# Kernel optimization log

Measured on AMD Instinct MI355X. Metric: run time of the kernel, lower is better.

The kernel has to match this reference:

```python
import jax, jax.numpy as jnp
import numpy as np

ROI = 7
NMS_THR = 0.01
NMS_SIZE = 100


def crop_and_resize(fmap, boxes, crop):
    # fmap [H,W,C], boxes [N,4] normalized (y1,x1,y2,x2) -> [N,crop,crop,C]
    H, W, C = fmap.shape
    t = jnp.linspace(0.0, 1.0, crop)
    ys = (boxes[:, 0:1] + (boxes[:, 2:3] - boxes[:, 0:1]) * t) * (H - 1)  # [N,crop]
    xs = (boxes[:, 1:2] + (boxes[:, 3:4] - boxes[:, 1:2]) * t) * (W - 1)
    y0 = jnp.clip(jnp.floor(ys), 0, H - 1).astype(jnp.int32)
    x0 = jnp.clip(jnp.floor(xs), 0, W - 1).astype(jnp.int32)
    y1 = jnp.clip(y0 + 1, 0, H - 1)
    x1 = jnp.clip(x0 + 1, 0, W - 1)
    wy = (ys - y0)[:, :, None, None]
    wx = (xs - x0)[:, None, :, None]
    Y0, Y1 = y0[:, :, None], y1[:, :, None]
    X0, X1 = x0[:, None, :], x1[:, None, :]
    f00 = fmap[Y0, X0]; f01 = fmap[Y0, X1]
    f10 = fmap[Y1, X0]; f11 = fmap[Y1, X1]
    return (f00 * (1 - wy) * (1 - wx) + f01 * (1 - wy) * wx
            + f10 * wy * (1 - wx) + f11 * wy * wx)


def iou_matrix(b):
    # b [N,4] (x1,y1,x2,y2)
    area = jnp.maximum(b[:, 2] - b[:, 0], 0) * jnp.maximum(b[:, 3] - b[:, 1], 0)
    lt = jnp.maximum(b[:, None, :2], b[None, :, :2])
    rb = jnp.minimum(b[:, None, 2:], b[None, :, 2:])
    wh = jnp.maximum(rb - lt, 0.0)
    inter = wh[..., 0] * wh[..., 1]
    return inter / (area[:, None] + area[None, :] - inter + 1e-8)


def nms(boxes, scores, thr, max_out):
    # greedy NMS, fixed-size output (pads with lowest-ranked boxes when fewer survive)
    N = boxes.shape[0]
    order = jnp.argsort(-scores)
    M = iou_matrix(boxes[order])
    idx = jnp.arange(N)
    def body(i, keep):
        sup = (M[i] > thr) & (idx > i) & keep[i]
        return keep & ~sup
    keep = jax.lax.fori_loop(0, N, body, jnp.ones(N, dtype=bool))
    rank = jnp.where(keep, idx, N + idx)
    sel = jnp.argsort(rank)[:max_out]
    return order[sel]


def make_boxes(key, n):
    kc, ks = jax.random.split(key)
    c = jax.random.uniform(kc, (n, 2), minval=0.1, maxval=0.9)
    s = jax.random.uniform(ks, (n, 2), minval=0.02, maxval=0.15)
    lo = jnp.clip(c - s / 2, 0.0, 1.0)
    hi = jnp.clip(c + s / 2, 0.0, 1.0)
    return jnp.concatenate([lo, hi], axis=1)  # (y1,x1,y2,x2)


def setup_inputs() -> dict:
    key = jax.random.key(0)
    ks = jax.random.split(key, 12)
    N, D, Hd = 1024, ROI * ROI * 32, 2048
    img_boxes = make_boxes(ks[0], N)
    bev_boxes = make_boxes(ks[1], N)
    bev_boxes_abs = bev_boxes[:, jnp.array([1, 0, 3, 2])] * 80.0  # (x1,y1,x2,y2) in meters
    def w(k, shape, fan_in):
        return jax.random.normal(k, shape, jnp.float32) * (2.0 / fan_in) ** 0.5
    return {
        'img_feat_map': jax.random.uniform(ks[2], (1, 360, 1200, 32), jnp.float32),
        'bev_feat_map': jax.random.uniform(ks[3], (1, 700, 800, 32), jnp.float32),
        'img_boxes': img_boxes,
        'bev_boxes': bev_boxes,
        'bev_boxes_abs': bev_boxes_abs,
        'img_mask': jnp.ones((1, 1, 1, 1), jnp.float32),
        'bev_mask': jnp.ones((1, 1, 1, 1), jnp.float32),
        'W1': w(ks[4], (D, Hd), D), 'b1': jnp.zeros((Hd,), jnp.float32),
        'W2': w(ks[5], (Hd, Hd), Hd), 'b2': jnp.zeros((Hd,), jnp.float32),
        'Wc': w(ks[6], (Hd, 2), Hd), 'bc': jnp.zeros((2,), jnp.float32),
        'Wo': w(ks[7], (Hd, 10), Hd), 'bo': jnp.zeros((10,), jnp.float32),
        'Wa': w(ks[8], (Hd, 2), Hd), 'ba': jnp.zeros((2,), jnp.float32),
    }


def reference(img_feat_map, bev_feat_map, img_boxes, bev_boxes, bev_boxes_abs,
              img_mask, bev_mask, W1, b1, W2, b2, Wc, bc, Wo, bo, Wa, ba):
    # ROI align on masked feature maps
    rois_rgb = crop_and_resize((img_mask * img_feat_map)[0], img_boxes, ROI)
    rois_bev = crop_and_resize((bev_mask * bev_feat_map)[0], bev_boxes, ROI)
    # mean fusion
    fused = (rois_rgb + rois_bev) / (img_mask + bev_mask)  # [N,7,7,32]
    # predictor
    x = fused.reshape(fused.shape[0], -1)
    h = jax.nn.relu(x @ W1 + b1)
    h = jax.nn.relu(h @ W2 + b2)
    obj = h @ Wc + bc            # [N,2]
    off = h @ Wo + bo            # [N,10]
    ang = h @ Wa + ba            # [N,2]
    obj_soft = jax.nn.softmax(obj, axis=1)
    orient = jnp.arctan2(ang[:, 1], ang[:, 0])  # convert_angle_to_orientation
    # offset-adjusted BEV boxes for NMS
    pb = bev_boxes_abs + 0.1 * off[:, :4]
    boxes = jnp.stack([jnp.minimum(pb[:, 0], pb[:, 2]), jnp.minimum(pb[:, 1], pb[:, 3]),
                       jnp.maximum(pb[:, 0], pb[:, 2]), jnp.maximum(pb[:, 1], pb[:, 3])], axis=1)
    scores = jnp.max(obj[:, 1:], axis=1)
    ti = nms(jax.lax.stop_gradient(boxes), jax.lax.stop_gradient(scores), NMS_THR, NMS_SIZE)
    # [100, 2 + 4 + 1]: softmax scores, pred bev boxes, orientations
    return jnp.concatenate([obj_soft[ti], boxes[ti], orient[ti][:, None]], axis=1)
```

## Files before the change

### kernel.cpp

```cpp
#include <hip/hip_runtime.h>
#include <math.h>

#define NBOX 1024
#define ROI_N 7
#define CH 32
#define FEAT (ROI_N*ROI_N*CH)
#define K1PAD 1600
#define HD 2048
#define NMS_THR_F 0.01f
#define NMS_OUT 100
#define MTRI_WORDS 8704

typedef _Float16 f16;
typedef f16 f16x8 __attribute__((ext_vector_type(8)));
typedef float f32x4 __attribute__((ext_vector_type(4)));

__device__ __forceinline__ void split_f16(float v, f16& h, f16& l) {
  h = (f16)v;
  l = (f16)((v - (float)h) * 4096.0f);
}

__global__ __launch_bounds__(256) void roi_fuse_kernel(
    const float* __restrict__ img, const float* __restrict__ bev,
    const float* __restrict__ img_boxes, const float* __restrict__ bev_boxes,
    const float* __restrict__ img_mask, const float* __restrict__ bev_mask,
    f16* __restrict__ xh, f16* __restrict__ xl)
{
  const int b = blockIdx.x;
  const float mi = img_mask[0], mb = bev_mask[0];
  const float denom = mi + mb;

  const float iy0 = img_boxes[b*4+0], ix0 = img_boxes[b*4+1];
  const float iy1 = img_boxes[b*4+2], ix1 = img_boxes[b*4+3];
  const float by0 = bev_boxes[b*4+0], bx0 = bev_boxes[b*4+1];
  const float by1 = bev_boxes[b*4+2], bx1 = bev_boxes[b*4+3];

  for (int idx = threadIdx.x; idx < K1PAD; idx += 256) {
    if (idx >= FEAT) {
      xh[(size_t)b*K1PAD + idx] = (f16)0.0f;
      xl[(size_t)b*K1PAD + idx] = (f16)0.0f;
      continue;
    }
    const int ti  = idx / (ROI_N*CH);
    const int rem = idx - ti*(ROI_N*CH);
    const int tj  = rem >> 5;
    const int c   = rem & 31;
    const float tt_i = (ti == ROI_N-1) ? 1.0f : ti * (1.0f/(ROI_N-1));
    const float tt_j = (tj == ROI_N-1) ? 1.0f : tj * (1.0f/(ROI_N-1));

    float vi, vb;
    {
      const int H = 360, W = 1200;
      const float ys = (iy0 + (iy1 - iy0) * tt_i) * (float)(H-1);
      const float xs = (ix0 + (ix1 - ix0) * tt_j) * (float)(W-1);
      int y0 = (int)floorf(ys); y0 = y0 < 0 ? 0 : (y0 > H-1 ? H-1 : y0);
      int x0 = (int)floorf(xs); x0 = x0 < 0 ? 0 : (x0 > W-1 ? W-1 : x0);
      const int y1 = (y0+1 > H-1) ? H-1 : y0+1;
      const int x1 = (x0+1 > W-1) ? W-1 : x0+1;
      const float wy = ys - (float)y0;
      const float wx = xs - (float)x0;
      const float f00 = img[(y0*W + x0)*CH + c];
      const float f01 = img[(y0*W + x1)*CH + c];
      const float f10 = img[(y1*W + x0)*CH + c];
      const float f11 = img[(y1*W + x1)*CH + c];
      vi = f00*(1.0f-wy)*(1.0f-wx) + f01*(1.0f-wy)*wx
         + f10*wy*(1.0f-wx)        + f11*wy*wx;
    }
    {
      const int H = 700, W = 800;
      const float ys = (by0 + (by1 - by0) * tt_i) * (float)(H-1);
      const float xs = (bx0 + (bx1 - bx0) * tt_j) * (float)(W-1);
      int y0 = (int)floorf(ys); y0 = y0 < 0 ? 0 : (y0 > H-1 ? H-1 : y0);
      int x0 = (int)floorf(xs); x0 = x0 < 0 ? 0 : (x0 > W-1 ? W-1 : x0);
      const int y1 = (y0+1 > H-1) ? H-1 : y0+1;
      const int x1 = (x0+1 > W-1) ? W-1 : x0+1;
      const float wy = ys - (float)y0;
      const float wx = xs - (float)x0;
      const float f00 = bev[(y0*W + x0)*CH + c];
      const float f01 = bev[(y0*W + x1)*CH + c];
      const float f10 = bev[(y1*W + x0)*CH + c];
      const float f11 = bev[(y1*W + x1)*CH + c];
      vb = f00*(1.0f-wy)*(1.0f-wx) + f01*(1.0f-wy)*wx
         + f10*wy*(1.0f-wx)        + f11*wy*wx;
    }
    f16 h, l;
    split_f16((mi*vi + mb*vb) / denom, h, l);
    xh[(size_t)b*K1PAD + idx] = h;
    xl[(size_t)b*K1PAD + idx] = l;
  }
}

__global__ __launch_bounds__(256) void convt_w_kernel(
    const float* __restrict__ W, f16* __restrict__ Wt_hi, f16* __restrict__ Wt_lo,
    int K, int Kpad, int N)
{
  __shared__ float t[64][33];
  const int tid = threadIdx.x;
  const int n0 = blockIdx.x * 32, k0 = blockIdx.y * 64;
#pragma unroll
  for (int p = 0; p < 8; ++p) {
    const int idx = tid + p*256;
    const int kk = idx >> 5, nn = idx & 31;
    const int k = k0 + kk;
    t[kk][nn] = (k < K) ? W[(size_t)k*N + n0 + nn] : 0.0f;
  }
  __syncthreads();
  const int nn = tid >> 3;
  const int kg = (tid & 7) * 8;
  f16x8 h8, l8;
#pragma unroll
  for (int q = 0; q < 8; ++q) {
    const float v = t[kg + q][nn];
    f16 h, l;
    split_f16(v, h, l);
    h8[q] = h; l8[q] = l;
  }
  *(f16x8*)&Wt_hi[(size_t)(n0+nn)*Kpad + k0 + kg] = h8;
  *(f16x8*)&Wt_lo[(size_t)(n0+nn)*Kpad + k0 + kg] = l8;
}

#define LOADG(KK)                                                              \
  do {                                                                         \
    _Pragma("unroll")                                                          \
    for (int j_ = 0; j_ < 2; ++j_) {                                           \
      const int ch_ = tid + j_*128;                                            \
      const int r_ = ch_ >> 2, c_ = (ch_ & 3) * 8;                             \
      pa_h[j_] = *(const f16x8*)&Ah_g[(size_t)(m0 + r_)*K + (KK) + c_];        \
      pa_l[j_] = *(const f16x8*)&Al_g[(size_t)(m0 + r_)*K + (KK) + c_];        \
    }                                                                          \
    _Pragma("unroll")                                                          \
    for (int j_ = 0; j_ < 4; ++j_) {                                           \
      const int ch_ = tid + j_*128;                                            \
      const int r_ = ch_ >> 2, c_ = (ch_ & 3) * 8;                             \
      pb_h[j_] = *(const f16x8*)&Bh_g[(size_t)(n0 + r_)*K + (KK) + c_];        \
      pb_l[j_] = *(const f16x8*)&Bl_g[(size_t)(n0 + r_)*K + (KK) + c_];        \
    }                                                                          \
  } while (0)

template<int SPLIT_OUT>
__global__ __launch_bounds__(128) void gemm_mfma(
    const f16* __restrict__ Ah_g, const f16* __restrict__ Al_g,
    const f16* __restrict__ Bh_g, const f16* __restrict__ Bl_g,
    const float* __restrict__ bias,
    float* __restrict__ Cf, f16* __restrict__ Ch, f16* __restrict__ Cl,
    int M, int N, int K)
{
  __shared__ f16 Ah[64][40], Al[64][40], Bh[128][40], Bl[128][40];
  const int tid = threadIdx.x;
  const int m0 = blockIdx.y * 64, n0 = blockIdx.x * 128;
  const int wn = tid >> 6, lane = tid & 63;
  const int frow = lane & 15, fkg = lane >> 4;

  f32x4 acc1[4][4], acc2[4][4];
#pragma unroll
  for (int i = 0; i < 4; ++i)
#pragma unroll
    for (int j = 0; j < 4; ++j)
#pragma unroll
      for (int r = 0; r < 4; ++r) { acc1[i][j][r] = 0.0f; acc2[i][j][r] = 0.0f; }

  f16x8 pa_h[2], pa_l[2], pb_h[4], pb_l[4];
  LOADG(0);

  for (int k0 = 0; k0 < K; k0 += 32) {
    __syncthreads();
#pragma unroll
    for (int j = 0; j < 2; ++j) {
      const int ch = tid + j*128, r = ch >> 2, c = (ch & 3) * 8;
      *(f16x8*)&Ah[r][c] = pa_h[j];
      *(f16x8*)&Al[r][c] = pa_l[j];
    }
#pragma unroll
    for (int j = 0; j < 4; ++j) {
      const int ch = tid + j*128, r = ch >> 2, c = (ch & 3) * 8;
      *(f16x8*)&Bh[r][c] = pb_h[j];
      *(f16x8*)&Bl[r][c] = pb_l[j];
    }
    __syncthreads();
    if (k0 + 32 < K) { LOADG(k0 + 32); }

    f16x8 bh[4], bl[4];
#pragma unroll
    for (int j = 0; j < 4; ++j) {
      bh[j] = *(const f16x8*)&Bh[wn*64 + j*16 + frow][fkg*8];
      bl[j] = *(const f16x8*)&Bl[wn*64 + j*16 + frow][fkg*8];
    }
#pragma unroll
    for (int i = 0; i < 4; ++i) {
      const f16x8 ah = *(const f16x8*)&Ah[i*16 + frow][fkg*8];
      const f16x8 al = *(const f16x8*)&Al[i*16 + frow][fkg*8];
#pragma unroll
      for (int j = 0; j < 4; ++j) {
        acc1[i][j] = __builtin_amdgcn_mfma_f32_16x16x32_f16(ah, bh[j], acc1[i][j], 0, 0, 0);
        acc2[i][j] = __builtin_amdgcn_mfma_f32_16x16x32_f16(ah, bl[j], acc2[i][j], 0, 0, 0);
        acc2[i][j] = __builtin_amdgcn_mfma_f32_16x16x32_f16(al, bh[j], acc2[i][j], 0, 0, 0);
      }
    }
  }

  const float s = 1.0f / 4096.0f;
#pragma unroll
  for (int i = 0; i < 4; ++i)
#pragma unroll
    for (int j = 0; j < 4; ++j) {
      const int col = n0 + wn*64 + j*16 + frow;
      const float bv = bias[col];
#pragma unroll
      for (int r = 0; r < 4; ++r) {
        const int row = m0 + i*16 + fkg*4 + r;
        float v = acc1[i][j][r] + acc2[i][j][r] * s + bv;
        v = fmaxf(v, 0.0f);
        if (SPLIT_OUT) {
          f16 h, l;
          split_f16(v, h, l);
          Ch[(size_t)row*N + col] = h;
          Cl[(size_t)row*N + col] = l;
        } else {
          Cf[(size_t)row*N + col] = v;
        }
      }
    }
}

__global__ __launch_bounds__(256) void heads_kernel(
    const float* __restrict__ h,
    const float* __restrict__ Wc, const float* __restrict__ bc,
    const float* __restrict__ Wo, const float* __restrict__ bo,
    const float* __restrict__ Wa, const float* __restrict__ ba,
    const float* __restrict__ bev_abs,
    float* __restrict__ obj_soft, float* __restrict__ boxes,
    float* __restrict__ orient, float* __restrict__ scores)
{
  const int r = blockIdx.x;
  const int tid = threadIdx.x;
  float acc[14];
#pragma unroll
  for (int j = 0; j < 14; ++j) acc[j] = 0.0f;
  for (int k = tid; k < HD; k += 256) {
    const float hv = h[(size_t)r*HD + k];
    acc[0]  += hv * Wc[k*2+0];
    acc[1]  += hv * Wc[k*2+1];
#pragma unroll
    for (int j = 0; j < 10; ++j) acc[2+j] += hv * Wo[k*10+j];
    acc[12] += hv * Wa[k*2+0];
    acc[13] += hv * Wa[k*2+1];
  }
  __shared__ float red[14][256];
#pragma unroll
  for (int j = 0; j < 14; ++j) red[j][tid] = acc[j];
  __syncthreads();
  for (int s = 128; s > 0; s >>= 1) {
    if (tid < s) {
#pragma unroll
      for (int j = 0; j < 14; ++j) red[j][tid] += red[j][tid + s];
    }
    __syncthreads();
  }
  if (tid == 0) {
    const float obj0 = red[0][0] + bc[0];
    const float obj1 = red[1][0] + bc[1];
    float off0 = red[2][0] + bo[0];
    float off1 = red[3][0] + bo[1];
    float off2 = red[4][0] + bo[2];
    float off3 = red[5][0] + bo[3];
    const float a0 = red[12][0] + ba[0];
    const float a1 = red[13][0] + ba[1];

    const float m  = fmaxf(obj0, obj1);
    const float e0 = expf(obj0 - m), e1 = expf(obj1 - m);
    const float se = e0 + e1;
    obj_soft[r*2+0] = e0 / se;
    obj_soft[r*2+1] = e1 / se;
    orient[r] = atan2f(a1, a0);

    const float pb0 = bev_abs[r*4+0] + 0.1f*off0;
    const float pb1 = bev_abs[r*4+1] + 0.1f*off1;
    const float pb2 = bev_abs[r*4+2] + 0.1f*off2;
    const float pb3 = bev_abs[r*4+3] + 0.1f*off3;
    boxes[r*4+0] = fminf(pb0, pb2);
    boxes[r*4+1] = fminf(pb1, pb3);
    boxes[r*4+2] = fmaxf(pb0, pb2);
    boxes[r*4+3] = fmaxf(pb1, pb3);
    scores[r] = obj1;
  }
}

__global__ __launch_bounds__(128) void sort_kernel(
    const float* __restrict__ scores, const float* __restrict__ boxes,
    int* __restrict__ order, float4* __restrict__ sboxes, float* __restrict__ sarea)
{
  const int i = blockIdx.x * 128 + threadIdx.x;
  const float my = scores[i];
  int pos = 0;
  for (int j = 0; j < NBOX; ++j) {
    const float sj = scores[j];
    pos += (sj > my) || (sj == my && j < i);
  }
  const float b0 = boxes[i*4+0], b1 = boxes[i*4+1];
  const float b2 = boxes[i*4+2], b3 = boxes[i*4+3];
  order[pos]  = i;
  sboxes[pos] = make_float4(b0, b1, b2, b3);
  sarea[pos]  = fmaxf(b2 - b0, 0.0f) * fmaxf(b3 - b1, 0.0f);
}

__device__ __forceinline__ int tri_base(int i) {
  const int b = i >> 6;
  return 64*(16*b - (b*(b-1))/2) + (i & 63)*(16 - b);
}

__global__ __launch_bounds__(256) void maskbuild_kernel(
    const float4* __restrict__ sboxes, const float* __restrict__ sarea,
    unsigned long long* __restrict__ Mtri)
{
  __shared__ float4 sb[NBOX];
  __shared__ float  sa[NBOX];
  const int tid = threadIdx.x;
  for (int t = tid; t < NBOX; t += 256) { sb[t] = sboxes[t]; sa[t] = sarea[t]; }
  __syncthreads();
  const int wv = tid >> 6, lane = tid & 63;
  for (int r = 0; r < 4; ++r) {
    const int i = blockIdx.x * 16 + wv * 4 + r;
    const float4 bi = sb[i];
    const float  ai = sa[i];
    const int b = i >> 6;
    const int base = tri_base(i);
    for (int w = b; w < 16; ++w) {
      const int j = w * 64 + lane;
      const float4 bj = sb[j];
      const float lt0 = fmaxf(bi.x, bj.x), lt1 = fmaxf(bi.y, bj.y);
      const float rb0 = fminf(bi.z, bj.z), rb1 = fminf(bi.w, bj.w);
      const float wq = fmaxf(rb0 - lt0, 0.0f), hq = fmaxf(rb1 - lt1, 0.0f);
      const float inter = wq * hq;
      const float iou = inter / (ai + sa[j] - inter + 1e-8f);
      const unsigned long long bits = __ballot((j > i) && (iou > NMS_THR_F));
      if (lane == 0) Mtri[base + (w - b)] = bits;
    }
  }
}

__global__ __launch_bounds__(1024) void scan_out_kernel(
    const unsigned long long* __restrict__ Mtri_g, const int* __restrict__ order,
    const float4* __restrict__ sboxes, const float* __restrict__ obj_soft,
    const float* __restrict__ orient, float* __restrict__ out)
{
  __shared__ unsigned long long M[MTRI_WORDS];
  __shared__ unsigned long long keepw[16];
  const int tid = threadIdx.x;
  for (int t = tid; t < MTRI_WORDS; t += 1024) M[t] = Mtri_g[t];
  __syncthreads();

  if (tid < 64) {
    const int lane = tid;
    unsigned long long kw = (lane < 16) ? ~0ull : 0ull;
    for (int w = 0; w < 16; ++w) {
      unsigned long long rem = __shfl(kw, w);
      while (rem) {
        const int bpos = __builtin_ctzll(rem);
        const int i = w * 64 + bpos;
        const int base = tri_base(i);
        unsigned long long m = 0;
        if (lane >= w && lane < 16) m = M[base + (lane - w)];
        kw &= ~m;
        const unsigned long long updated = __shfl(kw, w);
        rem = (bpos == 63) ? 0ull : (updated & (~0ull << (bpos + 1)));
      }
    }
    if (lane < 16) keepw[lane] = kw;
  }
  __syncthreads();

  const int w = tid >> 6, bpos = tid & 63;
  int pre = 0, total = 0;
#pragma unroll
  for (int q = 0; q < 16; ++q) {
    const int pc = __popcll(keepw[q]);
    total += pc;
    if (q < w) pre += pc;
  }
  pre += __popcll(keepw[w] & ((bpos == 0) ? 0ull : (~0ull >> (64 - bpos))));
  const int keep_self = (int)((keepw[w] >> bpos) & 1ull);
  const int rank = keep_self ? pre : (total + tid - pre);

  if (rank < NMS_OUT) {
    const int ob = order[tid];
    const float4 bx = sboxes[tid];
    out[rank*7+0] = obj_soft[ob*2+0];
    out[rank*7+1] = obj_soft[ob*2+1];
    out[rank*7+2] = bx.x;
    out[rank*7+3] = bx.y;
    out[rank*7+4] = bx.z;
    out[rank*7+5] = bx.w;
    out[rank*7+6] = orient[ob];
  }
}

extern "C" void kernel_launch(void* const* d_in, const int* in_sizes, int n_in,
                              void* d_out, int out_size, void* d_ws, size_t ws_size,
                              hipStream_t stream) {
  (void)in_sizes; (void)n_in; (void)out_size; (void)ws_size;
  const float* img       = (const float*)d_in[0];
  const float* bev       = (const float*)d_in[1];
  const float* img_boxes = (const float*)d_in[2];
  const float* bev_boxes = (const float*)d_in[3];
  const float* bev_abs   = (const float*)d_in[4];
  const float* img_mask  = (const float*)d_in[5];
  const float* bev_mask  = (const float*)d_in[6];
  const float* W1 = (const float*)d_in[7];
  const float* b1 = (const float*)d_in[8];
  const float* W2 = (const float*)d_in[9];
  const float* b2 = (const float*)d_in[10];
  const float* Wc = (const float*)d_in[11];
  const float* bc = (const float*)d_in[12];
  const float* Wo = (const float*)d_in[13];
  const float* bo = (const float*)d_in[14];
  const float* Wa = (const float*)d_in[15];
  const float* ba = (const float*)d_in[16];
  float* out = (float*)d_out;

  char* ws = (char*)d_ws;
  f16* xh    = (f16*)ws;                                  ws += (size_t)NBOX*K1PAD*2;
  f16* xl    = (f16*)ws;                                  ws += (size_t)NBOX*K1PAD*2;
  f16* h1h   = (f16*)ws;                                  ws += (size_t)NBOX*HD*2;
  f16* h1l   = (f16*)ws;                                  ws += (size_t)NBOX*HD*2;
  float* h2  = (float*)ws;                                ws += (size_t)NBOX*HD*4;
  f16* Wt1h  = (f16*)ws;                                  ws += (size_t)HD*K1PAD*2;
  f16* Wt1l  = (f16*)ws;                                  ws += (size_t)HD*K1PAD*2;
  f16* Wt2h  = (f16*)ws;                                  ws += (size_t)HD*HD*2;
  f16* Wt2l  = (f16*)ws;                                  ws += (size_t)HD*HD*2;
  float* obj_soft = (float*)ws;                           ws += NBOX*2*4;
  float* boxesf   = (float*)ws;                           ws += NBOX*4*4;
  float* orient   = (float*)ws;                           ws += NBOX*4;
  float* scores   = (float*)ws;                           ws += NBOX*4;
  int*   order    = (int*)ws;                             ws += NBOX*4;
  float4* sboxes  = (float4*)ws;                          ws += NBOX*16;
  float* sarea    = (float*)ws;                           ws += NBOX*4;
  unsigned long long* Mtri = (unsigned long long*)ws;

  roi_fuse_kernel<<<NBOX, 256, 0, stream>>>(img, bev, img_boxes, bev_boxes,
                                            img_mask, bev_mask, xh, xl);
  convt_w_kernel<<<dim3(HD/32, K1PAD/64), 256, 0, stream>>>(W1, Wt1h, Wt1l, FEAT, K1PAD, HD);
  convt_w_kernel<<<dim3(HD/32, HD/64),    256, 0, stream>>>(W2, Wt2h, Wt2l, HD, HD, HD);
  gemm_mfma<1><<<dim3(HD/128, NBOX/64), 128, 0, stream>>>(
      xh, xl, Wt1h, Wt1l, b1, (float*)nullptr, h1h, h1l, NBOX, HD, K1PAD);
  gemm_mfma<0><<<dim3(HD/128, NBOX/64), 128, 0, stream>>>(
      h1h, h1l, Wt2h, Wt2l, b2, h2, (f16*)nullptr, (f16*)nullptr, NBOX, HD, HD);
  heads_kernel<<<NBOX, 256, 0, stream>>>(h2, Wc, bc, Wo, bo, Wa, ba, bev_abs,
                                         obj_soft, boxesf, orient, scores);
  sort_kernel<<<8, 128, 0, stream>>>(scores, boxesf, order, sboxes, sarea);
  maskbuild_kernel<<<64, 256, 0, stream>>>(sboxes, sarea, Mtri);
  scan_out_kernel<<<1, 1024, 0, stream>>>(Mtri, order, sboxes, obj_soft, orient, out);
}
```

Baseline: 375.5 us.

## Split-K GEMMs with atomic accumulation, 128x128 tiles, XCD-aware mapping and LDS swizzle

Both MLP GEMMs become a 256-thread, 128x128-tile split-K kernel over 4 K chunks that accumulates with float atomics into bias-initialized fp32 buffers. The block index is mapped so tiles are grouped per XCD, and the LDS layout is XOR-swizzled to avoid bank conflicts. ReLU and the hi/lo fp16 split of the first layer's output move into the second GEMM's load path, and the second ReLU moves into the heads kernel. The aim is more parallelism and better occupancy, at the cost of atomic traffic, a bias-init pass, fp32 intermediates, and non-deterministic summation order.

```diff
diff --git a/kernel.cpp b/kernel.cpp
--- a/kernel.cpp
+++ b/kernel.cpp
@@ -5,7 +5,7 @@
 #define ROI_N 7
 #define CH 32
 #define FEAT (ROI_N*ROI_N*CH)
-#define K1PAD 1600
+#define K1PAD 1664
 #define HD 2048
 #define NMS_THR_F 0.01f
 #define NMS_OUT 100
@@ -119,37 +119,56 @@
   *(f16x8*)&Wt_lo[(size_t)(n0+nn)*Kpad + k0 + kg] = l8;
 }
 
-#define LOADG(KK)                                                              \
-  do {                                                                         \
-    _Pragma("unroll")                                                          \
-    for (int j_ = 0; j_ < 2; ++j_) {                                           \
-      const int ch_ = tid + j_*128;                                            \
-      const int r_ = ch_ >> 2, c_ = (ch_ & 3) * 8;                             \
-      pa_h[j_] = *(const f16x8*)&Ah_g[(size_t)(m0 + r_)*K + (KK) + c_];        \
-      pa_l[j_] = *(const f16x8*)&Al_g[(size_t)(m0 + r_)*K + (KK) + c_];        \
-    }                                                                          \
-    _Pragma("unroll")                                                          \
-    for (int j_ = 0; j_ < 4; ++j_) {                                           \
-      const int ch_ = tid + j_*128;                                            \
-      const int r_ = ch_ >> 2, c_ = (ch_ & 3) * 8;                             \
-      pb_h[j_] = *(const f16x8*)&Bh_g[(size_t)(n0 + r_)*K + (KK) + c_];        \
-      pb_l[j_] = *(const f16x8*)&Bl_g[(size_t)(n0 + r_)*K + (KK) + c_];        \
-    }                                                                          \
+__global__ __launch_bounds__(256) void init_bias_kernel(
+    const float* __restrict__ b1, const float* __restrict__ b2,
+    float4* __restrict__ h1f, float4* __restrict__ h2f)
+{
+  const int idx = blockIdx.x*256 + threadIdx.x;
+  const int c4 = idx & (HD/4 - 1);
+  h1f[idx] = *(const float4*)&b1[c4*4];
+  h2f[idx] = *(const float4*)&b2[c4*4];
+}
+
+#define STAGE_LOAD(KK)                                                          \
+  do {                                                                          \
+    _Pragma("unroll")                                                           \
+    for (int q_ = 0; q_ < 2; ++q_) {                                            \
+      const int ch_ = tid + q_*256;                                             \
+      const int r_ = ch_ >> 2, c_ = (ch_ & 3) * 8;                              \
+      if constexpr (AF32) {                                                     \
+        paf[q_][0] = *(const float4*)&Af_g[(size_t)(m0 + r_)*K + (KK) + c_];    \
+        paf[q_][1] = *(const float4*)&Af_g[(size_t)(m0 + r_)*K + (KK) + c_ + 4];\
+      } else {                                                                  \
+        pah[q_] = *(const f16x8*)&Ah_g[(size_t)(m0 + r_)*K + (KK) + c_];        \
+        pal[q_] = *(const f16x8*)&Al_g[(size_t)(m0 + r_)*K + (KK) + c_];        \
+      }                                                                         \
+      pbh[q_] = *(const f16x8*)&Bh_g[(size_t)(n0 + r_)*K + (KK) + c_];          \
+      pbl[q_] = *(const f16x8*)&Bl_g[(size_t)(n0 + r_)*K + (KK) + c_];          \
+    }                                                                           \
   } while (0)
 
-template<int SPLIT_OUT>
-__global__ __launch_bounds__(128) void gemm_mfma(
+template<int AF32>
+__global__ __launch_bounds__(256, 2) void gemm_sk(
     const f16* __restrict__ Ah_g, const f16* __restrict__ Al_g,
+    const float* __restrict__ Af_g,
     const f16* __restrict__ Bh_g, const f16* __restrict__ Bl_g,
-    const float* __restrict__ bias,
-    float* __restrict__ Cf, f16* __restrict__ Ch, f16* __restrict__ Cl,
-    int M, int N, int K)
-{
-  __shared__ f16 Ah[64][40], Al[64][40], Bh[128][40], Bl[128][40];
+    float* __restrict__ Cout, int M, int N, int K, int kchunk)
+{
+  __shared__ f16 Ah[128][32], Al[128][32], Bh[128][32], Bl[128][32];
   const int tid = threadIdx.x;
-  const int m0 = blockIdx.y * 64, n0 = blockIdx.x * 128;
-  const int wn = tid >> 6, lane = tid & 63;
+
+  const int g = blockIdx.x;
+  const int xcd = g & 7, c = g >> 3;
+  const int nb = xcd*2 + (c & 1);
+  const int mb = (c >> 1) & 7;
+  const int zb = c >> 4;
+  const int m0 = mb * 128, n0 = nb * 128;
+  const int kb = zb * kchunk, ke = kb + kchunk;
+
+  const int wid = tid >> 6, lane = tid & 63;
+  const int wr = wid >> 1, wc = wid & 1;
   const int frow = lane & 15, fkg = lane >> 4;
+  const int swz = (fkg ^ ((frow >> 1) & 3)) * 8;
 
   f32x4 acc1[4][4], acc2[4][4];
 #pragma unroll
@@ -159,36 +178,52 @@
 #pragma unroll
       for (int r = 0; r < 4; ++r) { acc1[i][j][r] = 0.0f; acc2[i][j][r] = 0.0f; }
 
-  f16x8 pa_h[2], pa_l[2], pb_h[4], pb_l[4];
-  LOADG(0);
-
-  for (int k0 = 0; k0 < K; k0 += 32) {
+  f16x8 pah[2], pal[2], pbh[2], pbl[2];
+  float4 paf[2][2];
+
+  STAGE_LOAD(kb);
+  for (int kk = kb; kk < ke; kk += 32) {
     __syncthreads();
 #pragma unroll
-    for (int j = 0; j < 2; ++j) {
-      const int ch = tid + j*128, r = ch >> 2, c = (ch & 3) * 8;
-      *(f16x8*)&Ah[r][c] = pa_h[j];
-      *(f16x8*)&Al[r][c] = pa_l[j];
-    }
+    for (int q = 0; q < 2; ++q) {
+      const int ch = tid + q*256;
+      const int r = ch >> 2, cs = ch & 3;
+      const int sl = (cs ^ ((r >> 1) & 3)) * 8;
+      if constexpr (AF32) {
+        const float4 a0 = paf[q][0], a1 = paf[q][1];
+        f16x8 hv, lv;
+        { float v = fmaxf(a0.x, 0.0f); f16 h,l; split_f16(v,h,l); hv[0]=h; lv[0]=l; }
+        { float v = fmaxf(a0.y, 0.0f); f16 h,l; split_f16(v,h,l); hv[1]=h; lv[1]=l; }
+        { float v = fmaxf(a0.z, 0.0f); f16 h,l; split_f16(v,h,l); hv[2]=h; lv[2]=l; }
+        { float v = fmaxf(a0.w, 0.0f); f16 h,l; split_f16(v,h,l); hv[3]=h; lv[3]=l; }
+        { float v = fmaxf(a1.x, 0.0f); f16 h,l; split_f16(v,h,l); hv[4]=h; lv[4]=l; }
+        { float v = fmaxf(a1.y, 0.0f); f16 h,l; split_f16(v,h,l); hv[5]=h; lv[5]=l; }
+        { float v = fmaxf(a1.z, 0.0f); f16 h,l; split_f16(v,h,l); hv[6]=h; lv[6]=l; }
+        { float v = fmaxf(a1.w, 0.0f); f16 h,l; split_f16(v,h,l); hv[7]=h; lv[7]=l; }
+        *(f16x8*)&Ah[r][sl] = hv;
+        *(f16x8*)&Al[r][sl] = lv;
+      } else {
+        *(f16x8*)&Ah[r][sl] = pah[q];
+        *(f16x8*)&Al[r][sl] = pal[q];
+      }
+      *(f16x8*)&Bh[r][sl] = pbh[q];
+      *(f16x8*)&Bl[r][sl] = pbl[q];
+    }
+    __syncthreads();
+    if (kk + 32 < ke) { STAGE_LOAD(kk + 32); }
+
+    f16x8 bh[4], bl[4];
 #pragma unroll
     for (int j = 0; j < 4; ++j) {
-      const int ch = tid + j*128, r = ch >> 2, c = (ch & 3) * 8;
-      *(f16x8*)&Bh[r][c] = pb_h[j];
-      *(f16x8*)&Bl[r][c] = pb_l[j];
-    }
-    __syncthreads();
-    if (k0 + 32 < K) { LOADG(k0 + 32); }
-
-    f16x8 bh[4], bl[4];
-#pragma unroll
-    for (int j = 0; j < 4; ++j) {
-      bh[j] = *(const f16x8*)&Bh[wn*64 + j*16 + frow][fkg*8];
-      bl[j] = *(const f16x8*)&Bl[wn*64 + j*16 + frow][fkg*8];
+      const int rr = wc*64 + j*16 + frow;
+      bh[j] = *(const f16x8*)&Bh[rr][swz];
+      bl[j] = *(const f16x8*)&Bl[rr][swz];
     }
 #pragma unroll
     for (int i = 0; i < 4; ++i) {
-      const f16x8 ah = *(const f16x8*)&Ah[i*16 + frow][fkg*8];
-      const f16x8 al = *(const f16x8*)&Al[i*16 + frow][fkg*8];
+      const int rr = wr*64 + i*16 + frow;
+      const f16x8 ah = *(const f16x8*)&Ah[rr][swz];
+      const f16x8 al = *(const f16x8*)&Al[rr][swz];
 #pragma unroll
       for (int j = 0; j < 4; ++j) {
         acc1[i][j] = __builtin_amdgcn_mfma_f32_16x16x32_f16(ah, bh[j], acc1[i][j], 0, 0, 0);
@@ -203,27 +238,17 @@
   for (int i = 0; i < 4; ++i)
 #pragma unroll
     for (int j = 0; j < 4; ++j) {
-      const int col = n0 + wn*64 + j*16 + frow;
-      const float bv = bias[col];
+      const int col = n0 + wc*64 + j*16 + frow;
 #pragma unroll
       for (int r = 0; r < 4; ++r) {
-        const int row = m0 + i*16 + fkg*4 + r;
-        float v = acc1[i][j][r] + acc2[i][j][r] * s + bv;
-        v = fmaxf(v, 0.0f);
-        if (SPLIT_OUT) {
-          f16 h, l;
-          split_f16(v, h, l);
-          Ch[(size_t)row*N + col] = h;
-          Cl[(size_t)row*N + col] = l;
-        } else {
-          Cf[(size_t)row*N + col] = v;
-        }
+        const int row = m0 + wr*64 + i*16 + fkg*4 + r;
+        atomicAdd(&Cout[(size_t)row*N + col], acc1[i][j][r] + acc2[i][j][r] * s);
       }
     }
 }
 
 __global__ __launch_bounds__(256) void heads_kernel(
-    const float* __restrict__ h,
+    const float* __restrict__ h2f,
     const float* __restrict__ Wc, const float* __restrict__ bc,
     const float* __restrict__ Wo, const float* __restrict__ bo,
     const float* __restrict__ Wa, const float* __restrict__ ba,
@@ -237,7 +262,7 @@
 #pragma unroll
   for (int j = 0; j < 14; ++j) acc[j] = 0.0f;
   for (int k = tid; k < HD; k += 256) {
-    const float hv = h[(size_t)r*HD + k];
+    const float hv = fmaxf(h2f[(size_t)r*HD + k], 0.0f);
     acc[0]  += hv * Wc[k*2+0];
     acc[1]  += hv * Wc[k*2+1];
 #pragma unroll
@@ -420,9 +445,8 @@
   char* ws = (char*)d_ws;
   f16* xh    = (f16*)ws;                                  ws += (size_t)NBOX*K1PAD*2;
   f16* xl    = (f16*)ws;                                  ws += (size_t)NBOX*K1PAD*2;
-  f16* h1h   = (f16*)ws;                                  ws += (size_t)NBOX*HD*2;
-  f16* h1l   = (f16*)ws;                                  ws += (size_t)NBOX*HD*2;
-  float* h2  = (float*)ws;                                ws += (size_t)NBOX*HD*4;
+  float* h1f = (float*)ws;                                ws += (size_t)NBOX*HD*4;
+  float* h2f = (float*)ws;                                ws += (size_t)NBOX*HD*4;
   f16* Wt1h  = (f16*)ws;                                  ws += (size_t)HD*K1PAD*2;
   f16* Wt1l  = (f16*)ws;                                  ws += (size_t)HD*K1PAD*2;
   f16* Wt2h  = (f16*)ws;                                  ws += (size_t)HD*HD*2;
@@ -438,13 +462,14 @@
 
   roi_fuse_kernel<<<NBOX, 256, 0, stream>>>(img, bev, img_boxes, bev_boxes,
                                             img_mask, bev_mask, xh, xl);
+  init_bias_kernel<<<NBOX*HD/4/256, 256, 0, stream>>>(b1, b2, (float4*)h1f, (float4*)h2f);
   convt_w_kernel<<<dim3(HD/32, K1PAD/64), 256, 0, stream>>>(W1, Wt1h, Wt1l, FEAT, K1PAD, HD);
   convt_w_kernel<<<dim3(HD/32, HD/64),    256, 0, stream>>>(W2, Wt2h, Wt2l, HD, HD, HD);
-  gemm_mfma<1><<<dim3(HD/128, NBOX/64), 128, 0, stream>>>(
-      xh, xl, Wt1h, Wt1l, b1, (float*)nullptr, h1h, h1l, NBOX, HD, K1PAD);
-  gemm_mfma<0><<<dim3(HD/128, NBOX/64), 128, 0, stream>>>(
-      h1h, h1l, Wt2h, Wt2l, b2, h2, (f16*)nullptr, (f16*)nullptr, NBOX, HD, HD);
-  heads_kernel<<<NBOX, 256, 0, stream>>>(h2, Wc, bc, Wo, bo, Wa, ba, bev_abs,
+  gemm_sk<0><<<512, 256, 0, stream>>>(xh, xl, (const float*)nullptr,
+                                      Wt1h, Wt1l, h1f, NBOX, HD, K1PAD, K1PAD/4);
+  gemm_sk<1><<<512, 256, 0, stream>>>((const f16*)nullptr, (const f16*)nullptr, h1f,
+                                      Wt2h, Wt2l, h2f, NBOX, HD, HD, HD/4);
+  heads_kernel<<<NBOX, 256, 0, stream>>>(h2f, Wc, bc, Wo, bo, Wa, ba, bev_abs,
                                          obj_soft, boxesf, orient, scores);
   sort_kernel<<<8, 128, 0, stream>>>(scores, boxesf, order, sboxes, sarea);
   maskbuild_kernel<<<64, 256, 0, stream>>>(sboxes, sarea, Mtri);
```

Measured after the change: 370.3 us. Within noise of the previous version (-1.4%).
